# Kernel optimization log

Measured on AMD Instinct MI355X. Metric: run time of the kernel, lower is better.

## Reference

```python
import jax, jax.numpy as jnp
import numpy as np

B, N, P, K, C = 8, 4096, 4096, 32, 128  # batch, points, npoint, neighbors, channels (=mlp[-1])
W_OUT = 16  # weightnet output channels (from Linear(16*mlp[-1], mlp[-1]))
EPS = 1e-5


def setup_inputs() -> dict:
    key = jax.random.key(0)
    ks = jax.random.split(key, 9)
    xyz = jax.random.normal(ks[0], (B, P, 3), jnp.float32)
    points = jax.random.normal(ks[1], (B, N, C), jnp.float32)
    local_coordinates = jax.random.normal(ks[2], (B, P, K, 3), jnp.float32)
    neighbor_lists = jax.random.randint(ks[3], (B, P, K), 0, N)
    data_idx = jax.random.randint(ks[4], (B,), 0, B)
    Ww = jax.random.normal(ks[5], (3, W_OUT), jnp.float32) * 0.1   # weightnet (pointwise linear 3->16)
    bw = jnp.zeros((W_OUT,), jnp.float32)
    Wl = jax.random.normal(ks[6], (W_OUT * C, C), jnp.float32) * 0.02  # nn.Linear(16*mlp[-1], mlp[-1])
    bl = jnp.zeros((C,), jnp.float32)
    gamma = jnp.ones((C,), jnp.float32)   # BatchNorm1d weight
    beta = jnp.zeros((C,), jnp.float32)   # BatchNorm1d bias
    return {"xyz": xyz, "points": points, "local_coordinates": local_coordinates,
            "neighbor_lists": neighbor_lists, "data_idx": data_idx,
            "Ww": Ww, "bw": bw, "Wl": Wl, "bl": bl, "gamma": gamma, "beta": beta}


def reference(xyz, points, local_coordinates, neighbor_lists, data_idx, Ww, bw, Wl, bl, gamma, beta):
    b, p, k, _ = local_coordinates.shape
    c = points.shape[-1]
    # weightnet: pointwise map of 3-D local coordinates to 16 weight channels -> [B,P,K,16]
    weights = local_coordinates @ Ww + bw
    # irregular neighbor gather: data[b,p,k,:] = points[b, neighbor_lists[b,p,k], :] -> [B,P,K,C]
    data = points[jnp.arange(b)[:, None, None], neighbor_lists]
    # per-point weighted aggregation over K neighbors: [B,P,C,16] -> flatten to [B,P,C*16]
    new_points = jnp.einsum('bpkc,bpkw->bpcw', data, weights).reshape(b, p, c * weights.shape[-1])
    # batch reindex via data_idx
    new_points = new_points[data_idx]
    # linear tail: [B,P,C]
    new_points = new_points @ Wl + bl
    # BatchNorm1d over channel dim (training-mode batch stats), then ReLU: [B,C,P]
    x = new_points.transpose(0, 2, 1)
    mean = x.mean(axis=(0, 2), keepdims=True)
    var = x.var(axis=(0, 2), keepdims=True)
    x = (x - mean) * jax.lax.rsqrt(var + EPS) * gamma[None, :, None] + beta[None, :, None]
    return xyz, jax.nn.relu(x)
```

## Files before the change

kernel.cpp:

```cpp
#include <hip/hip_runtime.h>

#define Bn 8
#define Nn 4096
#define Pn 4096
#define Kn 32
#define Cn 128

using float4v = __attribute__((ext_vector_type(4))) float;
using short8  = __attribute__((ext_vector_type(8))) short;

__device__ __forceinline__ unsigned short bf16b(float f) {
  union { float f; unsigned u; } v; v.f = f;
  unsigned r = v.u + 0x7FFFu + ((v.u >> 16) & 1u);
  return (unsigned short)(r >> 16);
}

__device__ __forceinline__ unsigned pkhi(float x, float y) {
  return __builtin_amdgcn_perm(__float_as_uint(y), __float_as_uint(x), 0x07060302u);
}

__global__ __launch_bounds__(256) void prep(const float* __restrict__ Wl,
                                            unsigned short* __restrict__ WlT,
                                            const float* __restrict__ xyz,
                                            float* __restrict__ out,
                                            float* __restrict__ gacc) {
  __shared__ unsigned short tile[128 * 130];
  const int t = threadIdx.x, blk = blockIdx.x;
  if (blk < 16) {
#pragma unroll
    for (int i = 0; i < 64; ++i) {
      int idx = i * 256 + t;
      int kl = idx >> 7, n = idx & 127;
      tile[n * 130 + kl] = bf16b(Wl[(size_t)(blk * 128 + kl) * 128 + n]);
    }
    __syncthreads();
#pragma unroll
    for (int i = 0; i < 64; ++i) {
      int idx = i * 256 + t;
      int n = idx >> 7, kl = idx & 127;
      WlT[(size_t)n * 2048 + blk * 128 + kl] = tile[n * 130 + kl];
    }
  } else {
    if (blk == 16) gacc[t] = 0.f;
    const int i0 = (blk - 16) * 3072 + t * 12;
#pragma unroll
    for (int i = 0; i < 3; ++i)
      *(float4v*)(out + i0 + i * 4) = *(const float4v*)(xyz + i0 + i * 4);
  }
}

__attribute__((amdgpu_waves_per_eu(4, 4)))
__global__ __launch_bounds__(256) void fused(
    const float* __restrict__ points, const float* __restrict__ lc,
    const int* __restrict__ nl, const int* __restrict__ didx,
    const float* __restrict__ Ww, const float* __restrict__ bwv,
    const unsigned short* __restrict__ WlT, const float* __restrict__ blv,
    float* __restrict__ xout, float* __restrict__ gacc) {
  __shared__ unsigned short Mlds[32 * 256];
  __shared__ int nlds[32 * 32];
  __shared__ float red[256];

  const int t = threadIdx.x, lane = t & 63, w = t >> 6;
  const int l15 = lane & 15, q = lane >> 4;
  const int b = blockIdx.x & 7;
  const int pg = blockIdx.x >> 3;
  const int p0 = pg * 32;
  const int db = didx[b];
  const char* __restrict__ pbase = (const char*)(points + (size_t)db * Nn * Cn);

  {
    int4 nv = *(const int4*)(nl + (size_t)(db * Pn + p0) * Kn + t * 4);
    nv.x <<= 9; nv.y <<= 9; nv.z <<= 9; nv.w <<= 9;
    *(int4*)&nlds[t * 4] = nv;
  }

  const float Ww0 = Ww[l15], Ww1 = Ww[16 + l15], Ww2 = Ww[32 + l15];
  const float bw0 = bwv[l15];

  short8 af[8];
#pragma unroll
  for (int i = 0; i < 8; ++i) {
    const int p = p0 + w * 8 + i;
    const int pk = (db * Pn + p) * Kn;
    const float* __restrict__ lcp = lc + (size_t)(pk + q * 8) * 3;
    float la[24];
#pragma unroll
    for (int v = 0; v < 6; ++v) *(float4v*)&la[v * 4] = *(const float4v*)(lcp + v * 4);
#pragma unroll
    for (int j = 0; j < 8; ++j) {
      float ww = bw0 + la[3 * j] * Ww0 + la[3 * j + 1] * Ww1 + la[3 * j + 2] * Ww2;
      af[i][j] = (short)bf16b(ww);
    }
  }

  float4v acc[2][2];
#pragma unroll
  for (int pt = 0; pt < 2; ++pt)
#pragma unroll
    for (int nt = 0; nt < 2; ++nt) acc[pt][nt] = (float4v){0.f, 0.f, 0.f, 0.f};

  __syncthreads();

  const unsigned short* __restrict__ bpt =
      WlT + (size_t)(w * 32 + l15) * 2048 + q * 8;
  const unsigned cvoff = (unsigned)(l15 * 4);

#define ISSUE(i, ct, fdst)                                                 \
  {                                                                        \
    const int pi_ = w * 8 + (i);                                           \
    int nk_[8];                                                            \
    *(int4*)&nk_[0] = *(const int4*)&nlds[pi_ * 32 + q * 8];               \
    *(int4*)&nk_[4] = *(const int4*)&nlds[pi_ * 32 + q * 8 + 4];           \
    _Pragma("unroll") for (int j = 0; j < 8; ++j)                          \
        fdst[j] = *(const float*)(pbase + ((unsigned)nk_[j] + cvoff +      \
                                           (unsigned)((ct) * 64)));        \
  }

#define FIN(i, fsrc)                                                       \
  {                                                                        \
    const int pi_ = w * 8 + (i);                                           \
    union { short8 s; unsigned u[4]; } bv_;                                \
    bv_.u[0] = pkhi(fsrc[0], fsrc[1]);                                     \
    bv_.u[1] = pkhi(fsrc[2], fsrc[3]);                                     \
    bv_.u[2] = pkhi(fsrc[4], fsrc[5]);                                     \
    bv_.u[3] = pkhi(fsrc[6], fsrc[7]);                                     \
    float4v d_ = {0.f, 0.f, 0.f, 0.f};                                     \
    d_ = __builtin_amdgcn_mfma_f32_16x16x32_bf16(af[i], bv_.s, d_, 0, 0, 0); \
    const unsigned off_ = (unsigned)(pi_ * 512 +                           \
        ((l15 * 32 + q * 8) ^ ((pi_ & 7) << 4)));                          \
    uint2 u_;                                                              \
    u_.x = pkhi(d_[0], d_[1]);                                             \
    u_.y = pkhi(d_[2], d_[3]);                                             \
    *(uint2*)((char*)Mlds + off_) = u_;                                    \
  }

  float fb[4][8];

  for (int ct = 0; ct < 8; ++ct) {
    ISSUE(0, ct, fb[0])
    ISSUE(1, ct, fb[1])
    ISSUE(2, ct, fb[2])
    ISSUE(3, ct, fb[3])
#pragma unroll
    for (int i = 0; i < 8; ++i) {
      FIN(i, fb[i & 3])
      if (i + 4 < 8) ISSUE(i + 4, ct, fb[i & 3])
    }
    __syncthreads();
    const unsigned short* __restrict__ bp = bpt + ct * 256;
#pragma unroll
    for (int ks = 0; ks < 8; ++ks) {
      const unsigned ax = (unsigned)((ks * 64 + q * 16) ^ ((l15 & 7) << 4));
      short8 a0 = *(const short8*)((const char*)Mlds + l15 * 512 + ax);
      short8 a1 = *(const short8*)((const char*)Mlds + (16 + l15) * 512 + ax);
      short8 b0 = *(const short8*)(bp + ks * 32);
      short8 b1 = *(const short8*)(bp + 32768 + ks * 32);
      acc[0][0] = __builtin_amdgcn_mfma_f32_16x16x32_bf16(a0, b0, acc[0][0], 0, 0, 0);
      acc[0][1] = __builtin_amdgcn_mfma_f32_16x16x32_bf16(a0, b1, acc[0][1], 0, 0, 0);
      acc[1][0] = __builtin_amdgcn_mfma_f32_16x16x32_bf16(a1, b0, acc[1][0], 0, 0, 0);
      acc[1][1] = __builtin_amdgcn_mfma_f32_16x16x32_bf16(a1, b1, acc[1][1], 0, 0, 0);
    }
    __syncthreads();
  }
#undef ISSUE
#undef FIN

#pragma unroll
  for (int nt = 0; nt < 2; ++nt) {
    const int ch = w * 32 + nt * 16 + l15;
    const float bb = blv[ch];
    float s = 0.f, sq = 0.f;
#pragma unroll
    for (int pt = 0; pt < 2; ++pt) {
      float4v o;
#pragma unroll
      for (int r = 0; r < 4; ++r) {
        float v = acc[pt][nt][r] + bb; o[r] = v; s += v; sq += v * v;
      }
      *(float4v*)(xout + ((size_t)(b * Cn + ch)) * Pn + p0 + pt * 16 + q * 4) = o;
    }
    s += __shfl_xor(s, 16); s += __shfl_xor(s, 32);
    sq += __shfl_xor(sq, 16); sq += __shfl_xor(sq, 32);
    if (lane < 16) { red[ch] = s; red[128 + ch] = sq; }
  }
  __syncthreads();
  atomicAdd(&gacc[t], red[t]);
}

__global__ __launch_bounds__(256) void finalize_ln(float* __restrict__ x,
                                                   const float* __restrict__ gacc,
                                                   const float* __restrict__ gamma,
                                                   const float* __restrict__ beta) {
  const int idx = blockIdx.x * 256 + threadIdx.x;
  const int fi = idx * 4;
  const int c = (fi >> 12) & 127;
  const float inv = 1.f / 32768.f;
  const float mean = gacc[c] * inv;
  const float var = gacc[128 + c] * inv - mean * mean;
  const float scale = rsqrtf(var + 1e-5f) * gamma[c];
  const float shift = beta[c] - mean * scale;
  float4v v = *(float4v*)(x + fi);
#pragma unroll
  for (int r = 0; r < 4; ++r) v[r] = fmaxf(v[r] * scale + shift, 0.f);
  *(float4v*)(x + fi) = v;
}

extern "C" void kernel_launch(void* const* d_in, const int* in_sizes, int n_in,
                              void* d_out, int out_size, void* d_ws, size_t ws_size,
                              hipStream_t stream) {
  const float* xyz    = (const float*)d_in[0];
  const float* points = (const float*)d_in[1];
  const float* lc     = (const float*)d_in[2];
  const int*   nl     = (const int*)d_in[3];
  const int*   didx   = (const int*)d_in[4];
  const float* Ww     = (const float*)d_in[5];
  const float* bw     = (const float*)d_in[6];
  const float* Wl     = (const float*)d_in[7];
  const float* bl     = (const float*)d_in[8];
  const float* gamma  = (const float*)d_in[9];
  const float* beta   = (const float*)d_in[10];

  float* out  = (float*)d_out;
  float* xout = out + (size_t)Bn * Pn * 3;
  unsigned short* WlT = (unsigned short*)d_ws;
  float* gacc = (float*)((char*)d_ws + (size_t)512 * 1024);

  prep<<<48, 256, 0, stream>>>(Wl, WlT, xyz, out, gacc);
  fused<<<1024, 256, 0, stream>>>(points, lc, nl, didx, Ww, bw, WlT, bl,
                                  xout, gacc);
  finalize_ln<<<4096, 256, 0, stream>>>(xout, gacc, gamma, beta);
}
```

Before: 193.2 us.

## Split fused kernel work across 8 waves per block and widen prep transpose grid

The fused kernel moves from 256 to 512 threads per block. Each of the 8 waves now handles 4 points and a 16-channel output slice instead of 8 points and 32 channels, so per-wave registers and gather buffers shrink and more waves are resident to hide gather latency. The Wl transpose prep is spread over 64 smaller tiles instead of 16. In exchange, each wave now does half the MFMA work per LDS stage, the gather software pipeline is shallower, and the block-level barriers now span more waves.

```diff
diff --git a/kernel.cpp b/kernel.cpp
--- a/kernel.cpp
+++ b/kernel.cpp
@@ -24,33 +24,32 @@
                                             const float* __restrict__ xyz,
                                             float* __restrict__ out,
                                             float* __restrict__ gacc) {
-  __shared__ unsigned short tile[128 * 130];
+  __shared__ unsigned short tile[128 * 33];
   const int t = threadIdx.x, blk = blockIdx.x;
-  if (blk < 16) {
-#pragma unroll
-    for (int i = 0; i < 64; ++i) {
+  if (blk < 64) {
+#pragma unroll
+    for (int i = 0; i < 16; ++i) {
       int idx = i * 256 + t;
       int kl = idx >> 7, n = idx & 127;
-      tile[n * 130 + kl] = bf16b(Wl[(size_t)(blk * 128 + kl) * 128 + n]);
+      tile[n * 33 + kl] = bf16b(Wl[(size_t)(blk * 32 + kl) * 128 + n]);
     }
     __syncthreads();
 #pragma unroll
-    for (int i = 0; i < 64; ++i) {
+    for (int i = 0; i < 16; ++i) {
       int idx = i * 256 + t;
-      int n = idx >> 7, kl = idx & 127;
-      WlT[(size_t)n * 2048 + blk * 128 + kl] = tile[n * 130 + kl];
+      int n = idx >> 5, kl = idx & 31;
+      WlT[(size_t)n * 2048 + blk * 32 + kl] = tile[n * 33 + kl];
     }
   } else {
-    if (blk == 16) gacc[t] = 0.f;
-    const int i0 = (blk - 16) * 3072 + t * 12;
+    if (blk == 64) gacc[t] = 0.f;
+    const int i0 = (blk - 64) * 3072 + t * 12;
 #pragma unroll
     for (int i = 0; i < 3; ++i)
       *(float4v*)(out + i0 + i * 4) = *(const float4v*)(xyz + i0 + i * 4);
   }
 }
 
-__attribute__((amdgpu_waves_per_eu(4, 4)))
-__global__ __launch_bounds__(256) void fused(
+__global__ __launch_bounds__(512, 8) void fused(
     const float* __restrict__ points, const float* __restrict__ lc,
     const int* __restrict__ nl, const int* __restrict__ didx,
     const float* __restrict__ Ww, const float* __restrict__ bwv,
@@ -69,18 +68,18 @@
   const char* __restrict__ pbase = (const char*)(points + (size_t)db * Nn * Cn);
 
   {
-    int4 nv = *(const int4*)(nl + (size_t)(db * Pn + p0) * Kn + t * 4);
-    nv.x <<= 9; nv.y <<= 9; nv.z <<= 9; nv.w <<= 9;
-    *(int4*)&nlds[t * 4] = nv;
+    int2 nv = *(const int2*)(nl + (size_t)(db * Pn + p0) * Kn + t * 2);
+    nv.x <<= 9; nv.y <<= 9;
+    *(int2*)&nlds[t * 2] = nv;
   }
 
   const float Ww0 = Ww[l15], Ww1 = Ww[16 + l15], Ww2 = Ww[32 + l15];
   const float bw0 = bwv[l15];
 
-  short8 af[8];
-#pragma unroll
-  for (int i = 0; i < 8; ++i) {
-    const int p = p0 + w * 8 + i;
+  short8 af[4];
+#pragma unroll
+  for (int i = 0; i < 4; ++i) {
+    const int p = p0 + w * 4 + i;
     const int pk = (db * Pn + p) * Kn;
     const float* __restrict__ lcp = lc + (size_t)(pk + q * 8) * 3;
     float la[24];
@@ -93,21 +92,19 @@
     }
   }
 
-  float4v acc[2][2];
-#pragma unroll
-  for (int pt = 0; pt < 2; ++pt)
-#pragma unroll
-    for (int nt = 0; nt < 2; ++nt) acc[pt][nt] = (float4v){0.f, 0.f, 0.f, 0.f};
+  float4v acc[2];
+  acc[0] = (float4v){0.f, 0.f, 0.f, 0.f};
+  acc[1] = (float4v){0.f, 0.f, 0.f, 0.f};
 
   __syncthreads();
 
-  const unsigned short* __restrict__ bpt =
-      WlT + (size_t)(w * 32 + l15) * 2048 + q * 8;
+  const unsigned short* __restrict__ bp =
+      WlT + (size_t)(w * 16 + l15) * 2048 + q * 8;
   const unsigned cvoff = (unsigned)(l15 * 4);
 
 #define ISSUE(i, ct, fdst)                                                 \
   {                                                                        \
-    const int pi_ = w * 8 + (i);                                           \
+    const int pi_ = w * 4 + (i);                                           \
     int nk_[8];                                                            \
     *(int4*)&nk_[0] = *(const int4*)&nlds[pi_ * 32 + q * 8];               \
     *(int4*)&nk_[4] = *(const int4*)&nlds[pi_ * 32 + q * 8 + 4];           \
@@ -118,7 +115,7 @@
 
 #define FIN(i, fsrc)                                                       \
   {                                                                        \
-    const int pi_ = w * 8 + (i);                                           \
+    const int pi_ = w * 4 + (i);                                           \
     union { short8 s; unsigned u[4]; } bv_;                                \
     bv_.u[0] = pkhi(fsrc[0], fsrc[1]);                                     \
     bv_.u[1] = pkhi(fsrc[2], fsrc[3]);                                     \
@@ -134,57 +131,51 @@
     *(uint2*)((char*)Mlds + off_) = u_;                                    \
   }
 
-  float fb[4][8];
+  float fb0[8], fb1[8];
 
   for (int ct = 0; ct < 8; ++ct) {
-    ISSUE(0, ct, fb[0])
-    ISSUE(1, ct, fb[1])
-    ISSUE(2, ct, fb[2])
-    ISSUE(3, ct, fb[3])
-#pragma unroll
-    for (int i = 0; i < 8; ++i) {
-      FIN(i, fb[i & 3])
-      if (i + 4 < 8) ISSUE(i + 4, ct, fb[i & 3])
-    }
+    ISSUE(0, ct, fb0)
+    ISSUE(1, ct, fb1)
+    FIN(0, fb0)
+    ISSUE(2, ct, fb0)
+    FIN(1, fb1)
+    ISSUE(3, ct, fb1)
+    FIN(2, fb0)
+    FIN(3, fb1)
     __syncthreads();
-    const unsigned short* __restrict__ bp = bpt + ct * 256;
 #pragma unroll
     for (int ks = 0; ks < 8; ++ks) {
       const unsigned ax = (unsigned)((ks * 64 + q * 16) ^ ((l15 & 7) << 4));
       short8 a0 = *(const short8*)((const char*)Mlds + l15 * 512 + ax);
       short8 a1 = *(const short8*)((const char*)Mlds + (16 + l15) * 512 + ax);
-      short8 b0 = *(const short8*)(bp + ks * 32);
-      short8 b1 = *(const short8*)(bp + 32768 + ks * 32);
-      acc[0][0] = __builtin_amdgcn_mfma_f32_16x16x32_bf16(a0, b0, acc[0][0], 0, 0, 0);
-      acc[0][1] = __builtin_amdgcn_mfma_f32_16x16x32_bf16(a0, b1, acc[0][1], 0, 0, 0);
-      acc[1][0] = __builtin_amdgcn_mfma_f32_16x16x32_bf16(a1, b0, acc[1][0], 0, 0, 0);
-      acc[1][1] = __builtin_amdgcn_mfma_f32_16x16x32_bf16(a1, b1, acc[1][1], 0, 0, 0);
+      short8 b0 = *(const short8*)(bp + ct * 256 + ks * 32);
+      acc[0] = __builtin_amdgcn_mfma_f32_16x16x32_bf16(a0, b0, acc[0], 0, 0, 0);
+      acc[1] = __builtin_amdgcn_mfma_f32_16x16x32_bf16(a1, b0, acc[1], 0, 0, 0);
     }
     __syncthreads();
   }
 #undef ISSUE
 #undef FIN
 
-#pragma unroll
-  for (int nt = 0; nt < 2; ++nt) {
-    const int ch = w * 32 + nt * 16 + l15;
+  {
+    const int ch = w * 16 + l15;
     const float bb = blv[ch];
     float s = 0.f, sq = 0.f;
 #pragma unroll
-    for (int pt = 0; pt < 2; ++pt) {
+    for (int rt = 0; rt < 2; ++rt) {
       float4v o;
 #pragma unroll
       for (int r = 0; r < 4; ++r) {
-        float v = acc[pt][nt][r] + bb; o[r] = v; s += v; sq += v * v;
+        float v = acc[rt][r] + bb; o[r] = v; s += v; sq += v * v;
       }
-      *(float4v*)(xout + ((size_t)(b * Cn + ch)) * Pn + p0 + pt * 16 + q * 4) = o;
+      *(float4v*)(xout + ((size_t)(b * Cn + ch)) * Pn + p0 + rt * 16 + q * 4) = o;
     }
     s += __shfl_xor(s, 16); s += __shfl_xor(s, 32);
     sq += __shfl_xor(sq, 16); sq += __shfl_xor(sq, 32);
     if (lane < 16) { red[ch] = s; red[128 + ch] = sq; }
   }
   __syncthreads();
-  atomicAdd(&gacc[t], red[t]);
+  if (t < 256) atomicAdd(&gacc[t], red[t]);
 }
 
 __global__ __launch_bounds__(256) void finalize_ln(float* __restrict__ x,
@@ -225,8 +216,8 @@
   unsigned short* WlT = (unsigned short*)d_ws;
   float* gacc = (float*)((char*)d_ws + (size_t)512 * 1024);
 
-  prep<<<48, 256, 0, stream>>>(Wl, WlT, xyz, out, gacc);
-  fused<<<1024, 256, 0, stream>>>(points, lc, nl, didx, Ww, bw, WlT, bl,
+  prep<<<96, 256, 0, stream>>>(Wl, WlT, xyz, out, gacc);
+  fused<<<1024, 512, 0, stream>>>(points, lc, nl, didx, Ww, bw, WlT, bl,
                                   xout, gacc);
   finalize_ln<<<4096, 256, 0, stream>>>(xout, gacc, gamma, beta);
 }
```

New measurement: 203.5 us. 5.3% more time.
